# Kernel tuning notes

Measured on AMD Instinct MI355X. Metric: run time of the kernel, lower is better.

## Reference

```python
import jax, jax.numpy as jnp
import numpy as np

B, S, D_MODEL, D_K, D_V = 8, 2048, 1024, 512, 512


def setup_inputs() -> dict:
    key = jax.random.key(0)
    ks = jax.random.split(key, 7)
    sq = jax.random.normal(ks[0], (B, S, D_MODEL), dtype=jnp.float32)
    skv = jax.random.normal(ks[1], (B, S, D_MODEL), dtype=jnp.float32)
    q_pad = jax.random.uniform(ks[2], (B, S)) < 0.1
    kv_pad = jax.random.uniform(ks[3], (B, S)) < 0.1
    Wq = jax.random.normal(ks[4], (D_MODEL, D_K), dtype=jnp.float32) * (D_MODEL ** -0.5)
    Wk = jax.random.normal(ks[5], (D_MODEL, D_K), dtype=jnp.float32) * (D_MODEL ** -0.5)
    Wv = jax.random.normal(ks[6], (D_MODEL, D_V), dtype=jnp.float32) * (D_MODEL ** -0.5)
    return {
        "source_query": sq,
        "source_key_value": skv,
        "source_query_padding_mask": q_pad,
        "source_key_value_padding_mask": kv_pad,
        "Wq": Wq,
        "Wk": Wk,
        "Wv": Wv,
    }


def reference(source_query, source_key_value, source_query_padding_mask,
              source_key_value_padding_mask, Wq, Wk, Wv):
    neg_inf = jnp.float32(-jnp.inf)
    q = source_query @ Wq          # [B,Sq,d_k]
    k = source_key_value @ Wk      # [B,Sk,d_k]
    v = source_key_value @ Wv      # [B,Sk,d_v]
    scale = jnp.float32(D_K) ** -0.5
    scores = jnp.einsum("bqd,bkd->bqk", q, k) * scale  # [B,Sq,Sk]
    # query padding mask broadcast along key dim, kv padding mask along query dim
    pad = source_query_padding_mask[:, :, None] | source_key_value_padding_mask[:, None, :]
    scores = jnp.where(pad, neg_inf, scores)
    # causal mask (masked=True): positions above diagonal blocked
    Sq = scores.shape[1]
    causal = jnp.tril(jnp.ones((Sq, Sq), dtype=bool))
    scores = jnp.where(causal[None, :, :], scores, neg_inf)
    attn = jax.nn.softmax(scores, axis=-1)
    # fully-masked rows produce NaN -> zero (matches torch nan masked_fill)
    attn = jnp.where(jnp.isnan(attn), jnp.float32(0.0), attn)
    # dropout p=0.0 (eval): identity
    out = jnp.einsum("bqk,bkv->bqv", attn, v)  # [B,Sq,d_v]
    return out
```

## Files before the change

kernel.cpp:

```cpp
#include <hip/hip_runtime.h>

typedef unsigned short u16;
typedef unsigned int   u32;
typedef __attribute__((ext_vector_type(4))) float  f32x4;
typedef __attribute__((ext_vector_type(8))) __bf16 bf16x8;

#define BATCH 8
#define SEQ   2048
#define DMODEL 1024
#define DK    512
#define DV    512
#define SCALE 0.044194173824159216f

__device__ __forceinline__ u16 f2bf(float f) {
  u32 u = __float_as_uint(f);
  return (u16)((u + 0x7fffu + ((u >> 16) & 1u)) >> 16);
}

__device__ __forceinline__ bool read_mask(const void* p, int idx, int mode) {
  if (mode == 1) return ((const unsigned char*)p)[idx] != 0;
  if (mode == 2) return ((const float*)p)[idx] != 0.0f;
  return ((const int*)p)[idx] != 0;
}

__device__ __forceinline__ void gl_lds16(const u16* g, u16* l) {
  __builtin_amdgcn_global_load_lds(
      (const __attribute__((address_space(1))) u32*)g,
      (__attribute__((address_space(3))) u32*)l, 16, 0, 0);
}

__global__ void detect_mode(const int* __restrict__ qp, int* __restrict__ flag) {
  __shared__ int f;
  if (threadIdx.x == 0) f = 0;
  __syncthreads();
  int local = 0;
  for (int i = threadIdx.x; i < 4096; i += 256) {
    int v = qp[i];
    if (v == 0x3F800000) local |= 2;
    else if (v != 0 && v != 1 && v != -1) local |= 1;
  }
  if (local) atomicOr(&f, local);
  __syncthreads();
  if (threadIdx.x == 0) {
    int m = 0;
    if (f & 2) m = 2; else if (f & 1) m = 1;
    *flag = m;
  }
}

__global__ __launch_bounds__(256) void wt_transpose(const float* __restrict__ W0,
                                                    const float* __restrict__ W1,
                                                    const float* __restrict__ W2,
                                                    u16* __restrict__ dst) {
  const float* W = (blockIdx.z == 0) ? W0 : (blockIdx.z == 1) ? W1 : W2;
  u16* out = dst + (size_t)blockIdx.z * (DK * DMODEL);
  __shared__ float T[32][33];
  int k0 = blockIdx.x * 32, n0 = blockIdx.y * 32;
  int tx = threadIdx.x, ty = threadIdx.y;
#pragma unroll
  for (int i = 0; i < 4; ++i) {
    int r = ty + i * 8;
    T[r][tx] = W[(size_t)(k0 + r) * DK + n0 + tx];
  }
  __syncthreads();
#pragma unroll
  for (int i = 0; i < 4; ++i) {
    int r = ty + i * 8;
    out[(size_t)(n0 + r) * DMODEL + k0 + tx] = f2bf(T[tx][r]);
  }
}

__global__ __launch_bounds__(256) void convert_bf16(const float* __restrict__ src,
                                                    u16* __restrict__ dst) {
  int i = (blockIdx.x * 256 + threadIdx.x) * 8;
  f32x4 a = *(const f32x4*)(src + i);
  f32x4 b = *(const f32x4*)(src + i + 4);
  uint4 o;
  o.x = (u32)f2bf(a[0]) | ((u32)f2bf(a[1]) << 16);
  o.y = (u32)f2bf(a[2]) | ((u32)f2bf(a[3]) << 16);
  o.z = (u32)f2bf(b[0]) | ((u32)f2bf(b[1]) << 16);
  o.w = (u32)f2bf(b[2]) | ((u32)f2bf(b[3]) << 16);
  *(uint4*)(dst + i) = o;
}

__global__ __launch_bounds__(256, 3) void proj_gemm(const u16* __restrict__ A,
                                                    const u16* __restrict__ Wt_base,
                                                    int z0, u16* __restrict__ dst0,
                                                    u16* __restrict__ dst1) {
  int z = z0 + blockIdx.z;
  const u16* Wt = Wt_base + (size_t)z * (DK * DMODEL);
  u16* dst = (z == 2) ? dst1 : dst0;
  int n0 = blockIdx.x * 128, m0 = blockIdx.y * 128;

  __shared__ __align__(16) u16 As[128 * 64];
  __shared__ __align__(16) u16 Bs[128 * 64];

  int tid = threadIdx.x, lane = tid & 63, w = tid >> 6;
  int wm = w & 1, wn = w >> 1;
  int l15 = lane & 15, lg = lane >> 4;
  int r3 = lane >> 3, c7 = lane & 7;
  int csw = c7 ^ r3;

  f32x4 acc[4][4];
#pragma unroll
  for (int m = 0; m < 4; ++m)
#pragma unroll
    for (int n = 0; n < 4; ++n) acc[m][n] = (f32x4)0.0f;

  for (int k0 = 0; k0 < DMODEL; k0 += 64) {
    __syncthreads();
#pragma unroll
    for (int u = 0; u < 4; ++u) {
      int t = w * 4 + u;
      gl_lds16(A  + (size_t)(m0 + t * 8 + r3) * DMODEL + k0 + csw * 8, &As[t * 512]);
      gl_lds16(Wt + (size_t)(n0 + t * 8 + r3) * DMODEL + k0 + csw * 8, &Bs[t * 512]);
    }
    __syncthreads();
#pragma unroll
    for (int ks = 0; ks < 2; ++ks) {
      bf16x8 af[4], bfv[4];
#pragma unroll
      for (int m = 0; m < 4; ++m) {
        int row = wm * 64 + m * 16 + l15;
        af[m] = *(const bf16x8*)&As[row * 64 + (((ks * 4 + lg) ^ (l15 & 7)) * 8)];
      }
#pragma unroll
      for (int n = 0; n < 4; ++n) {
        int row = wn * 64 + n * 16 + l15;
        bfv[n] = *(const bf16x8*)&Bs[row * 64 + (((ks * 4 + lg) ^ (l15 & 7)) * 8)];
      }
#pragma unroll
      for (int m = 0; m < 4; ++m)
#pragma unroll
        for (int n = 0; n < 4; ++n)
          acc[m][n] = __builtin_amdgcn_mfma_f32_16x16x32_bf16(af[m], bfv[n], acc[m][n], 0, 0, 0);
    }
  }

  if (z != 2) {
#pragma unroll
    for (int m = 0; m < 4; ++m) {
      int rowb = m0 + wm * 64 + m * 16;
#pragma unroll
      for (int n = 0; n < 4; ++n) {
        int col = n0 + wn * 64 + n * 16 + l15;
        size_t base = (size_t)(rowb >> 4) * 8192 + (size_t)(col >> 5) * 512 + (col & 31);
#pragma unroll
        for (int r = 0; r < 4; ++r)
          dst[base + (lg * 4 + r) * 32] = f2bf(acc[m][n][r]);
      }
    }
  } else {
#pragma unroll
    for (int m = 0; m < 4; ++m) {
      int row0 = m0 + wm * 64 + m * 16 + lg * 4;
      int b = row0 >> 11, s0 = row0 & 2047;
#pragma unroll
      for (int n = 0; n < 4; ++n) {
        int dv = n0 + wn * 64 + n * 16 + l15;
        size_t off = (size_t)b * (SEQ * DV) + (size_t)(dv >> 4) * 32768 +
                     (size_t)(s0 >> 5) * 512 + (dv & 15) * 32 + (s0 & 31);
        u16 tmp[4] __attribute__((aligned(8)));
#pragma unroll
        for (int r = 0; r < 4; ++r) tmp[r] = f2bf(acc[m][n][r]);
        *(uint2*)&dst[off] = *(const uint2*)tmp;
      }
    }
  }
}

__global__ __launch_bounds__(512, 4) void attn_kernel(
    const u16* __restrict__ Qf, const u16* __restrict__ Kf,
    const u16* __restrict__ Vf, const void* __restrict__ qpad,
    const void* __restrict__ kvpad, const int* __restrict__ flag,
    float* __restrict__ out) {
  __shared__ __align__(16) u16 Qs[32 * 512];
  __shared__ __align__(16) u16 Pbuf[32 * 72];
  __shared__ float partm[32 * 4];
  __shared__ float partl[32 * 4];

  int tid = threadIdx.x;
  int lane = tid & 63, w = tid >> 6;
  int l15 = lane & 15, lg = lane >> 4;
  int wk = w & 3;
  int m  = w >> 2;
  int bi = blockIdx.x;
  int b = bi & 7, j = bi >> 3;
  int c = j & 31, h = j >> 5;
  int qt = ((c ^ h) & 1) ? (63 - c) : c;
  int q0 = qt * 32;
  int mode = *flag;
  int lanoff = l15 * 32 + lg * 8;

  const u16* Qb = Qf + (size_t)b * (SEQ * DK);
  const u16* Kb = Kf + (size_t)b * (SEQ * DK);
  const u16* Vb = Vf + (size_t)b * (SEQ * DV);

  {
    const u16* qsrc = Qb + (size_t)qt * 16384 + lane * 8;
#pragma unroll
    for (int u = 0; u < 4; ++u) {
      int i = w * 4 + u;
      gl_lds16(qsrc + i * 512, &Qs[i * 512]);
    }
  }

  f32x4 o[2][4];
#pragma unroll
  for (int mf = 0; mf < 2; ++mf)
#pragma unroll
    for (int n = 0; n < 4; ++n) o[mf][n] = (f32x4)0.0f;

  float mo[2][4], lsum[4];
#pragma unroll
  for (int mf = 0; mf < 2; ++mf)
#pragma unroll
    for (int r = 0; r < 4; ++r) mo[mf][r] = -1e38f;
#pragma unroll
  for (int r = 0; r < 4; ++r) lsum[r] = 0.0f;

  int nkt = (q0 + 95) >> 6;
  __syncthreads();

  for (int kt = 0; kt < nkt; ++kt) {
    int k0 = kt * 64;
    int key = k0 + wk * 16 + l15;
    bool kvm = read_mask(kvpad, b * SEQ + key, mode);

    f32x4 sa = (f32x4)0.0f, sb = (f32x4)0.0f;
    {
      const u16* kp = Kb + (size_t)((k0 >> 4) + wk) * 8192 + lanoff;
      const u16* qp = &Qs[m * 8192 + lanoff];
#pragma unroll
      for (int ks = 0; ks < 16; ks += 2) {
        bf16x8 qv0 = *(const bf16x8*)(qp + ks * 512);
        bf16x8 kv0 = *(const bf16x8*)(kp + ks * 512);
        bf16x8 qv1 = *(const bf16x8*)(qp + (ks + 1) * 512);
        bf16x8 kv1 = *(const bf16x8*)(kp + (ks + 1) * 512);
        sa = __builtin_amdgcn_mfma_f32_16x16x32_bf16(qv0, kv0, sa, 0, 0, 0);
        sb = __builtin_amdgcn_mfma_f32_16x16x32_bf16(qv1, kv1, sb, 0, 0, 0);
      }
    }

    float sv[4];
#pragma unroll
    for (int r = 0; r < 4; ++r) {
      int qrow = q0 + m * 16 + lg * 4 + r;
      float x = (sa[r] + sb[r]) * SCALE;
      sv[r] = (kvm || key > qrow) ? -__builtin_inff() : x;
    }

    float wmax[4];
#pragma unroll
    for (int r = 0; r < 4; ++r) wmax[r] = sv[r];
#pragma unroll
    for (int d = 1; d < 16; d <<= 1)
#pragma unroll
      for (int r = 0; r < 4; ++r) wmax[r] = fmaxf(wmax[r], __shfl_xor(wmax[r], d));
    if (l15 == 0) {
#pragma unroll
      for (int r = 0; r < 4; ++r) partm[(m * 16 + lg * 4 + r) * 4 + wk] = wmax[r];
    }
    __syncthreads();

    float al[2][4];
#pragma unroll
    for (int mf = 0; mf < 2; ++mf)
#pragma unroll
      for (int r = 0; r < 4; ++r) {
        int row = mf * 16 + lg * 4 + r;
        float tm = fmaxf(fmaxf(partm[row * 4 + 0], partm[row * 4 + 1]),
                         fmaxf(partm[row * 4 + 2], partm[row * 4 + 3]));
        float mn = fmaxf(mo[mf][r], fmaxf(tm, -1e38f));
        al[mf][r] = __expf(mo[mf][r] - mn);
        mo[mf][r] = mn;
      }
    float ws[4];
#pragma unroll
    for (int r = 0; r < 4; ++r) {
      int row = m * 16 + lg * 4 + r;
      float p = __expf(sv[r] - mo[m][r]);
      Pbuf[row * 72 + wk * 16 + l15] = f2bf(p);
      ws[r] = p;
    }
#pragma unroll
    for (int d = 1; d < 16; d <<= 1)
#pragma unroll
      for (int r = 0; r < 4; ++r) ws[r] += __shfl_xor(ws[r], d);
#pragma unroll
    for (int r = 0; r < 4; ++r) lsum[r] = lsum[r] * al[m][r] + ws[r];
    __syncthreads();

#pragma unroll
    for (int mf = 0; mf < 2; ++mf)
#pragma unroll
      for (int n = 0; n < 4; ++n)
#pragma unroll
        for (int r = 0; r < 4; ++r) o[mf][n][r] *= al[mf][r];

    {
      bf16x8 pa0[2], pa1[2];
#pragma unroll
      for (int ks = 0; ks < 2; ++ks) {
        pa0[ks] = *(const bf16x8*)&Pbuf[l15 * 72 + ks * 32 + lg * 8];
        pa1[ks] = *(const bf16x8*)&Pbuf[(16 + l15) * 72 + ks * 32 + lg * 8];
      }
      const u16* vp = Vb + (size_t)(w * 4) * 32768 + (size_t)(k0 >> 5) * 512 + lanoff;
#pragma unroll
      for (int n = 0; n < 4; ++n) {
#pragma unroll
        for (int ks = 0; ks < 2; ++ks) {
          bf16x8 bv = *(const bf16x8*)(vp + (size_t)n * 32768 + ks * 512);
          o[0][n] = __builtin_amdgcn_mfma_f32_16x16x32_bf16(pa0[ks], bv, o[0][n], 0, 0, 0);
          o[1][n] = __builtin_amdgcn_mfma_f32_16x16x32_bf16(pa1[ks], bv, o[1][n], 0, 0, 0);
        }
      }
    }
  }

  if (l15 == 0) {
#pragma unroll
    for (int r = 0; r < 4; ++r) partl[(m * 16 + lg * 4 + r) * 4 + wk] = lsum[r];
  }
  __syncthreads();
  {
    float f[2][4];
#pragma unroll
    for (int mf = 0; mf < 2; ++mf)
#pragma unroll
      for (int r = 0; r < 4; ++r) {
        int row = mf * 16 + lg * 4 + r;
        float l = partl[row * 4 + 0] + partl[row * 4 + 1] +
                  partl[row * 4 + 2] + partl[row * 4 + 3];
        bool qp = read_mask(qpad, b * SEQ + q0 + row, mode);
        f[mf][r] = (l > 0.0f && !qp) ? 1.0f / l : 0.0f;
      }
#pragma unroll
    for (int mf = 0; mf < 2; ++mf)
#pragma unroll
      for (int n = 0; n < 4; ++n) {
        int dv = w * 64 + n * 16 + l15;
#pragma unroll
        for (int r = 0; r < 4; ++r) {
          int row = mf * 16 + lg * 4 + r;
          out[(size_t)(b * SEQ + q0 + row) * DV + dv] = o[mf][n][r] * f[mf][r];
        }
      }
  }
}

extern "C" void kernel_launch(void* const* d_in, const int* in_sizes, int n_in,
                              void* d_out, int out_size, void* d_ws, size_t ws_size,
                              hipStream_t stream) {
  const float* sq  = (const float*)d_in[0];
  const float* skv = (const float*)d_in[1];
  const void* qp   = d_in[2];
  const void* kvp  = d_in[3];
  const float* Wq  = (const float*)d_in[4];
  const float* Wk  = (const float*)d_in[5];
  const float* Wv  = (const float*)d_in[6];
  char* ws = (char*)d_ws;

  u16* Abf = (u16*)ws;
  u16* Qf  = (u16*)(ws + 33554432);
  u16* Kf  = (u16*)(ws + 50331648);
  u16* Vf  = (u16*)(ws + 67108864);
  u16* Wt  = (u16*)(ws + 83886080);
  int* flag = (int*)(ws + 87031808);

  wt_transpose<<<dim3(32, 16, 3), dim3(32, 8, 1), 0, stream>>>(Wq, Wk, Wv, Wt);
  detect_mode<<<1, 256, 0, stream>>>((const int*)qp, flag);

  convert_bf16<<<8192, 256, 0, stream>>>(sq, Abf);
  proj_gemm<<<dim3(4, 128, 1), dim3(256), 0, stream>>>(Abf, Wt, 0, Qf, Qf);

  convert_bf16<<<8192, 256, 0, stream>>>(skv, Abf);
  proj_gemm<<<dim3(4, 128, 2), dim3(256), 0, stream>>>(Abf, Wt, 1, Kf, Vf);

  attn_kernel<<<dim3(512), dim3(512), 0, stream>>>(Qf, Kf, Vf, qp, kvp, flag,
                                                   (float*)d_out);
}
```

Baseline: 447.6 us.

## Restructure attention into 1024-thread blocks with 128-key tiles and paired query tiles

Block size goes from 512 to 1024 threads, and the grid halves to 256 blocks. Each block now processes two query tiles, (63-c) then c, in two passes to balance causal work. Key tiles grow from 64 to 128 keys, split over 8 waves, and Q fragments are held in registers instead of staged in LDS. The aim is to halve the number of barrier-separated iterations per query tile and drop the Q shared-memory round trip. The cost is much higher register pressure (16 bf16x8 Q fragments per lane), only 256 blocks which may underfill the CUs, and more masked work on the diagonal tile.

```diff
diff --git a/kernel.cpp b/kernel.cpp
--- a/kernel.cpp
+++ b/kernel.cpp
@@ -169,26 +169,24 @@
   }
 }
 
-__global__ __launch_bounds__(512, 4) void attn_kernel(
+__global__ __launch_bounds__(1024) void attn_kernel(
     const u16* __restrict__ Qf, const u16* __restrict__ Kf,
     const u16* __restrict__ Vf, const void* __restrict__ qpad,
     const void* __restrict__ kvpad, const int* __restrict__ flag,
     float* __restrict__ out) {
-  __shared__ __align__(16) u16 Qs[32 * 512];
-  __shared__ __align__(16) u16 Pbuf[32 * 72];
-  __shared__ float partm[32 * 4];
-  __shared__ float partl[32 * 4];
+  __shared__ __align__(16) u16 Pbuf[32 * 136];
+  __shared__ __align__(16) float partm[32 * 8];
+  __shared__ __align__(16) float partl[32 * 8];
 
   int tid = threadIdx.x;
   int lane = tid & 63, w = tid >> 6;
   int l15 = lane & 15, lg = lane >> 4;
-  int wk = w & 3;
-  int m  = w >> 2;
+  int wk = w & 7;
+  int mS = w >> 3;
+  int mf = w & 1;
+  int dq = w >> 1;
   int bi = blockIdx.x;
-  int b = bi & 7, j = bi >> 3;
-  int c = j & 31, h = j >> 5;
-  int qt = ((c ^ h) & 1) ? (63 - c) : c;
-  int q0 = qt * 32;
+  int b = bi & 7, c = bi >> 3;
   int mode = *flag;
   int lanoff = l15 * 32 + lg * 8;
 
@@ -196,156 +194,156 @@
   const u16* Kb = Kf + (size_t)b * (SEQ * DK);
   const u16* Vb = Vf + (size_t)b * (SEQ * DV);
 
-  {
-    const u16* qsrc = Qb + (size_t)qt * 16384 + lane * 8;
-#pragma unroll
-    for (int u = 0; u < 4; ++u) {
-      int i = w * 4 + u;
-      gl_lds16(qsrc + i * 512, &Qs[i * 512]);
-    }
-  }
-
-  f32x4 o[2][4];
-#pragma unroll
-  for (int mf = 0; mf < 2; ++mf)
-#pragma unroll
-    for (int n = 0; n < 4; ++n) o[mf][n] = (f32x4)0.0f;
-
-  float mo[2][4], lsum[4];
-#pragma unroll
-  for (int mf = 0; mf < 2; ++mf)
-#pragma unroll
-    for (int r = 0; r < 4; ++r) mo[mf][r] = -1e38f;
-#pragma unroll
-  for (int r = 0; r < 4; ++r) lsum[r] = 0.0f;
-
-  int nkt = (q0 + 95) >> 6;
-  __syncthreads();
-
-  for (int kt = 0; kt < nkt; ++kt) {
-    int k0 = kt * 64;
-    int key = k0 + wk * 16 + l15;
-    bool kvm = read_mask(kvpad, b * SEQ + key, mode);
-
-    f32x4 sa = (f32x4)0.0f, sb = (f32x4)0.0f;
+#pragma unroll 1
+  for (int pass = 0; pass < 2; ++pass) {
+    int qt = pass ? c : (63 - c);
+    int q0 = qt * 32;
+
+    bf16x8 qf[16];
     {
-      const u16* kp = Kb + (size_t)((k0 >> 4) + wk) * 8192 + lanoff;
-      const u16* qp = &Qs[m * 8192 + lanoff];
-#pragma unroll
-      for (int ks = 0; ks < 16; ks += 2) {
-        bf16x8 qv0 = *(const bf16x8*)(qp + ks * 512);
-        bf16x8 kv0 = *(const bf16x8*)(kp + ks * 512);
-        bf16x8 qv1 = *(const bf16x8*)(qp + (ks + 1) * 512);
-        bf16x8 kv1 = *(const bf16x8*)(kp + (ks + 1) * 512);
-        sa = __builtin_amdgcn_mfma_f32_16x16x32_bf16(qv0, kv0, sa, 0, 0, 0);
-        sb = __builtin_amdgcn_mfma_f32_16x16x32_bf16(qv1, kv1, sb, 0, 0, 0);
-      }
-    }
-
-    float sv[4];
-#pragma unroll
-    for (int r = 0; r < 4; ++r) {
-      int qrow = q0 + m * 16 + lg * 4 + r;
-      float x = (sa[r] + sb[r]) * SCALE;
-      sv[r] = (kvm || key > qrow) ? -__builtin_inff() : x;
-    }
-
-    float wmax[4];
-#pragma unroll
-    for (int r = 0; r < 4; ++r) wmax[r] = sv[r];
-#pragma unroll
-    for (int d = 1; d < 16; d <<= 1)
-#pragma unroll
-      for (int r = 0; r < 4; ++r) wmax[r] = fmaxf(wmax[r], __shfl_xor(wmax[r], d));
+      const u16* qp = Qb + (size_t)(qt * 2 + mS) * 8192 + lanoff;
+#pragma unroll
+      for (int ks = 0; ks < 16; ++ks) qf[ks] = *(const bf16x8*)(qp + ks * 512);
+    }
+
+    f32x4 o[4];
+#pragma unroll
+    for (int n = 0; n < 4; ++n) o[n] = (f32x4)0.0f;
+
+    float mo[2][4], lsum[4];
+#pragma unroll
+    for (int mfi = 0; mfi < 2; ++mfi)
+#pragma unroll
+      for (int r = 0; r < 4; ++r) mo[mfi][r] = -1e38f;
+#pragma unroll
+    for (int r = 0; r < 4; ++r) lsum[r] = 0.0f;
+
+    int nkt = (q0 + 159) >> 7;
+
+    for (int kt = 0; kt < nkt; ++kt) {
+      int k0 = kt << 7;
+      int key = k0 + wk * 16 + l15;
+      bool kvm = read_mask(kvpad, b * SEQ + key, mode);
+
+      f32x4 sa = (f32x4)0.0f, sb = (f32x4)0.0f;
+      {
+        const u16* kp = Kb + (size_t)(kt * 8 + wk) * 8192 + lanoff;
+#pragma unroll
+        for (int ks = 0; ks < 16; ks += 2) {
+          bf16x8 kv0 = *(const bf16x8*)(kp + ks * 512);
+          bf16x8 kv1 = *(const bf16x8*)(kp + (ks + 1) * 512);
+          sa = __builtin_amdgcn_mfma_f32_16x16x32_bf16(qf[ks], kv0, sa, 0, 0, 0);
+          sb = __builtin_amdgcn_mfma_f32_16x16x32_bf16(qf[ks + 1], kv1, sb, 0, 0, 0);
+        }
+      }
+
+      float sv[4];
+#pragma unroll
+      for (int r = 0; r < 4; ++r) {
+        int qrow = q0 + mS * 16 + lg * 4 + r;
+        float x = (sa[r] + sb[r]) * SCALE;
+        sv[r] = (kvm || key > qrow) ? -__builtin_inff() : x;
+      }
+
+      float wmax[4];
+#pragma unroll
+      for (int r = 0; r < 4; ++r) wmax[r] = sv[r];
+#pragma unroll
+      for (int d = 1; d < 16; d <<= 1)
+#pragma unroll
+        for (int r = 0; r < 4; ++r) wmax[r] = fmaxf(wmax[r], __shfl_xor(wmax[r], d));
+      if (l15 == 0) {
+#pragma unroll
+        for (int r = 0; r < 4; ++r) partm[(mS * 16 + lg * 4 + r) * 8 + wk] = wmax[r];
+      }
+      __syncthreads();
+
+      float al[2][4];
+#pragma unroll
+      for (int mfi = 0; mfi < 2; ++mfi)
+#pragma unroll
+        for (int r = 0; r < 4; ++r) {
+          int row = mfi * 16 + lg * 4 + r;
+          f32x4 p0 = *(const f32x4*)&partm[row * 8];
+          f32x4 p1 = *(const f32x4*)&partm[row * 8 + 4];
+          float tm = fmaxf(fmaxf(fmaxf(p0[0], p0[1]), fmaxf(p0[2], p0[3])),
+                           fmaxf(fmaxf(p1[0], p1[1]), fmaxf(p1[2], p1[3])));
+          float mn = fmaxf(mo[mfi][r], fmaxf(tm, -1e38f));
+          al[mfi][r] = __expf(mo[mfi][r] - mn);
+          mo[mfi][r] = mn;
+        }
+      float ws[4];
+#pragma unroll
+      for (int r = 0; r < 4; ++r) {
+        int row = mS * 16 + lg * 4 + r;
+        float mS_m = mS ? mo[1][r] : mo[0][r];
+        float p = __expf(sv[r] - mS_m);
+        Pbuf[row * 136 + wk * 16 + l15] = f2bf(p);
+        ws[r] = p;
+      }
+#pragma unroll
+      for (int d = 1; d < 16; d <<= 1)
+#pragma unroll
+        for (int r = 0; r < 4; ++r) ws[r] += __shfl_xor(ws[r], d);
+#pragma unroll
+      for (int r = 0; r < 4; ++r) {
+        float alS = mS ? al[1][r] : al[0][r];
+        lsum[r] = lsum[r] * alS + ws[r];
+      }
+      __syncthreads();
+
+#pragma unroll
+      for (int n = 0; n < 4; ++n)
+#pragma unroll
+        for (int r = 0; r < 4; ++r) {
+          float alF = mf ? al[1][r] : al[0][r];
+          o[n][r] *= alF;
+        }
+
+      {
+        bf16x8 pa[4];
+#pragma unroll
+        for (int ks = 0; ks < 4; ++ks)
+          pa[ks] = *(const bf16x8*)&Pbuf[(mf * 16 + l15) * 136 + ks * 32 + lg * 8];
+        const u16* vp = Vb + (size_t)(dq * 4) * 32768 + (size_t)(kt * 4) * 512 + lanoff;
+#pragma unroll
+        for (int n = 0; n < 4; ++n) {
+#pragma unroll
+          for (int ks = 0; ks < 4; ++ks) {
+            bf16x8 bv = *(const bf16x8*)(vp + (size_t)n * 32768 + ks * 512);
+            o[n] = __builtin_amdgcn_mfma_f32_16x16x32_bf16(pa[ks], bv, o[n], 0, 0, 0);
+          }
+        }
+      }
+    }
+
     if (l15 == 0) {
 #pragma unroll
-      for (int r = 0; r < 4; ++r) partm[(m * 16 + lg * 4 + r) * 4 + wk] = wmax[r];
+      for (int r = 0; r < 4; ++r) partl[(mS * 16 + lg * 4 + r) * 8 + wk] = lsum[r];
     }
     __syncthreads();
-
-    float al[2][4];
-#pragma unroll
-    for (int mf = 0; mf < 2; ++mf)
+    {
+      float f[4];
 #pragma unroll
       for (int r = 0; r < 4; ++r) {
         int row = mf * 16 + lg * 4 + r;
-        float tm = fmaxf(fmaxf(partm[row * 4 + 0], partm[row * 4 + 1]),
-                         fmaxf(partm[row * 4 + 2], partm[row * 4 + 3]));
-        float mn = fmaxf(mo[mf][r], fmaxf(tm, -1e38f));
-        al[mf][r] = __expf(mo[mf][r] - mn);
-        mo[mf][r] = mn;
-      }
-    float ws[4];
-#pragma unroll
-    for (int r = 0; r < 4; ++r) {
-      int row = m * 16 + lg * 4 + r;
-      float p = __expf(sv[r] - mo[m][r]);
-      Pbuf[row * 72 + wk * 16 + l15] = f2bf(p);
-      ws[r] = p;
-    }
-#pragma unroll
-    for (int d = 1; d < 16; d <<= 1)
-#pragma unroll
-      for (int r = 0; r < 4; ++r) ws[r] += __shfl_xor(ws[r], d);
-#pragma unroll
-    for (int r = 0; r < 4; ++r) lsum[r] = lsum[r] * al[m][r] + ws[r];
-    __syncthreads();
-
-#pragma unroll
-    for (int mf = 0; mf < 2; ++mf)
-#pragma unroll
-      for (int n = 0; n < 4; ++n)
-#pragma unroll
-        for (int r = 0; r < 4; ++r) o[mf][n][r] *= al[mf][r];
-
-    {
-      bf16x8 pa0[2], pa1[2];
-#pragma unroll
-      for (int ks = 0; ks < 2; ++ks) {
-        pa0[ks] = *(const bf16x8*)&Pbuf[l15 * 72 + ks * 32 + lg * 8];
-        pa1[ks] = *(const bf16x8*)&Pbuf[(16 + l15) * 72 + ks * 32 + lg * 8];
-      }
-      const u16* vp = Vb + (size_t)(w * 4) * 32768 + (size_t)(k0 >> 5) * 512 + lanoff;
+        f32x4 a = *(const f32x4*)&partl[row * 8];
+        f32x4 b2 = *(const f32x4*)&partl[row * 8 + 4];
+        float l = (a[0] + a[1] + a[2] + a[3]) + (b2[0] + b2[1] + b2[2] + b2[3]);
+        bool qp = read_mask(qpad, b * SEQ + q0 + row, mode);
+        f[r] = (l > 0.0f && !qp) ? 1.0f / l : 0.0f;
+      }
 #pragma unroll
       for (int n = 0; n < 4; ++n) {
-#pragma unroll
-        for (int ks = 0; ks < 2; ++ks) {
-          bf16x8 bv = *(const bf16x8*)(vp + (size_t)n * 32768 + ks * 512);
-          o[0][n] = __builtin_amdgcn_mfma_f32_16x16x32_bf16(pa0[ks], bv, o[0][n], 0, 0, 0);
-          o[1][n] = __builtin_amdgcn_mfma_f32_16x16x32_bf16(pa1[ks], bv, o[1][n], 0, 0, 0);
-        }
-      }
-    }
-  }
-
-  if (l15 == 0) {
-#pragma unroll
-    for (int r = 0; r < 4; ++r) partl[(m * 16 + lg * 4 + r) * 4 + wk] = lsum[r];
-  }
-  __syncthreads();
-  {
-    float f[2][4];
-#pragma unroll
-    for (int mf = 0; mf < 2; ++mf)
-#pragma unroll
-      for (int r = 0; r < 4; ++r) {
-        int row = mf * 16 + lg * 4 + r;
-        float l = partl[row * 4 + 0] + partl[row * 4 + 1] +
-                  partl[row * 4 + 2] + partl[row * 4 + 3];
-        bool qp = read_mask(qpad, b * SEQ + q0 + row, mode);
-        f[mf][r] = (l > 0.0f && !qp) ? 1.0f / l : 0.0f;
-      }
-#pragma unroll
-    for (int mf = 0; mf < 2; ++mf)
-#pragma unroll
-      for (int n = 0; n < 4; ++n) {
-        int dv = w * 64 + n * 16 + l15;
+        int dv = dq * 64 + n * 16 + l15;
 #pragma unroll
         for (int r = 0; r < 4; ++r) {
           int row = mf * 16 + lg * 4 + r;
-          out[(size_t)(b * SEQ + q0 + row) * DV + dv] = o[mf][n][r] * f[mf][r];
-        }
-      }
+          out[(size_t)(b * SEQ + q0 + row) * DV + dv] = o[n][r] * f[r];
+        }
+      }
+    }
+    __syncthreads();
   }
 }
 
@@ -377,6 +375,6 @@
   convert_bf16<<<8192, 256, 0, stream>>>(skv, Abf);
   proj_gemm<<<dim3(4, 128, 2), dim3(256), 0, stream>>>(Abf, Wt, 1, Kf, Vf);
 
-  attn_kernel<<<dim3(512), dim3(512), 0, stream>>>(Qf, Kf, Vf, qp, kvp, flag,
-                                                   (float*)d_out);
-}
+  attn_kernel<<<dim3(256), dim3(1024), 0, stream>>>(Qf, Kf, Vf, qp, kvp, flag,
+                                                    (float*)d_out);
+}
```

Measured after the change: 538.5 us. 1.2x slower.

## Pair causal query tiles per block and swizzle Q in LDS, prefetch V

Applied to the files above, without the earlier changes.

The attention kernel now launches 256 blocks, and each block processes two query tiles in sequence, a long one (63-c) and then a short one (c), so every block does an equal amount of causal work. Q is loaded into LDS with an XOR swizzle to reduce bank conflicts, and V fragments are loaded into registers right after the QK MFMAs so their latency overlaps the softmax. The rescale factor is computed once per row and shared through LDS instead of being computed redundantly, and the partial max/sum reads use vector LDS loads. With half the blocks on a 256-CU part, occupancy and latency hiding may drop.

```diff
diff --git a/kernel.cpp b/kernel.cpp
--- a/kernel.cpp
+++ b/kernel.cpp
@@ -176,176 +176,187 @@
     float* __restrict__ out) {
   __shared__ __align__(16) u16 Qs[32 * 512];
   __shared__ __align__(16) u16 Pbuf[32 * 72];
-  __shared__ float partm[32 * 4];
-  __shared__ float partl[32 * 4];
+  __shared__ __align__(16) float partm[32 * 4];
+  __shared__ __align__(16) float partl[32 * 4];
+  __shared__ __align__(16) float ald[32];
 
   int tid = threadIdx.x;
   int lane = tid & 63, w = tid >> 6;
   int l15 = lane & 15, lg = lane >> 4;
   int wk = w & 3;
-  int m  = w >> 2;
+  int mS = w >> 2;
   int bi = blockIdx.x;
-  int b = bi & 7, j = bi >> 3;
-  int c = j & 31, h = j >> 5;
-  int qt = ((c ^ h) & 1) ? (63 - c) : c;
-  int q0 = qt * 32;
+  int b = bi & 7, c = bi >> 3;
   int mode = *flag;
   int lanoff = l15 * 32 + lg * 8;
+  int qswz = (((l15 * 4 + lg) ^ (l15 >> 1)) * 8);
+  int sswz = ((lane ^ ((lane >> 3) & 7)) * 8);
 
   const u16* Qb = Qf + (size_t)b * (SEQ * DK);
   const u16* Kb = Kf + (size_t)b * (SEQ * DK);
   const u16* Vb = Vf + (size_t)b * (SEQ * DV);
 
-  {
-    const u16* qsrc = Qb + (size_t)qt * 16384 + lane * 8;
-#pragma unroll
-    for (int u = 0; u < 4; ++u) {
-      int i = w * 4 + u;
-      gl_lds16(qsrc + i * 512, &Qs[i * 512]);
-    }
-  }
-
-  f32x4 o[2][4];
-#pragma unroll
-  for (int mf = 0; mf < 2; ++mf)
-#pragma unroll
-    for (int n = 0; n < 4; ++n) o[mf][n] = (f32x4)0.0f;
-
-  float mo[2][4], lsum[4];
-#pragma unroll
-  for (int mf = 0; mf < 2; ++mf)
-#pragma unroll
-    for (int r = 0; r < 4; ++r) mo[mf][r] = -1e38f;
-#pragma unroll
-  for (int r = 0; r < 4; ++r) lsum[r] = 0.0f;
-
-  int nkt = (q0 + 95) >> 6;
-  __syncthreads();
-
-  for (int kt = 0; kt < nkt; ++kt) {
-    int k0 = kt * 64;
-    int key = k0 + wk * 16 + l15;
-    bool kvm = read_mask(kvpad, b * SEQ + key, mode);
-
-    f32x4 sa = (f32x4)0.0f, sb = (f32x4)0.0f;
+#pragma unroll 1
+  for (int pass = 0; pass < 2; ++pass) {
+    int qt = pass ? c : (63 - c);
+    int q0 = qt * 32;
+
     {
-      const u16* kp = Kb + (size_t)((k0 >> 4) + wk) * 8192 + lanoff;
-      const u16* qp = &Qs[m * 8192 + lanoff];
-#pragma unroll
-      for (int ks = 0; ks < 16; ks += 2) {
-        bf16x8 qv0 = *(const bf16x8*)(qp + ks * 512);
-        bf16x8 kv0 = *(const bf16x8*)(kp + ks * 512);
-        bf16x8 qv1 = *(const bf16x8*)(qp + (ks + 1) * 512);
-        bf16x8 kv1 = *(const bf16x8*)(kp + (ks + 1) * 512);
-        sa = __builtin_amdgcn_mfma_f32_16x16x32_bf16(qv0, kv0, sa, 0, 0, 0);
-        sb = __builtin_amdgcn_mfma_f32_16x16x32_bf16(qv1, kv1, sb, 0, 0, 0);
-      }
-    }
-
-    float sv[4];
-#pragma unroll
-    for (int r = 0; r < 4; ++r) {
-      int qrow = q0 + m * 16 + lg * 4 + r;
-      float x = (sa[r] + sb[r]) * SCALE;
-      sv[r] = (kvm || key > qrow) ? -__builtin_inff() : x;
-    }
-
-    float wmax[4];
-#pragma unroll
-    for (int r = 0; r < 4; ++r) wmax[r] = sv[r];
-#pragma unroll
-    for (int d = 1; d < 16; d <<= 1)
-#pragma unroll
-      for (int r = 0; r < 4; ++r) wmax[r] = fmaxf(wmax[r], __shfl_xor(wmax[r], d));
+      const u16* qsrc = Qb + (size_t)qt * 16384 + sswz;
+#pragma unroll
+      for (int u = 0; u < 8; ++u) {
+        int i = w * 8 + u;
+        gl_lds16(qsrc + i * 512, &Qs[i * 512]);
+      }
+    }
+
+    f32x4 o[2][4];
+#pragma unroll
+    for (int mf = 0; mf < 2; ++mf)
+#pragma unroll
+      for (int n = 0; n < 4; ++n) o[mf][n] = (f32x4)0.0f;
+
+    float mo[4], lsum[4];
+#pragma unroll
+    for (int r = 0; r < 4; ++r) { mo[r] = -1e38f; lsum[r] = 0.0f; }
+
+    int nkt = (q0 + 95) >> 6;
+    __syncthreads();
+
+    for (int kt = 0; kt < nkt; ++kt) {
+      int key = (kt << 6) + wk * 16 + l15;
+      bool kvm = read_mask(kvpad, b * SEQ + key, mode);
+
+      f32x4 sa = (f32x4)0.0f, sb = (f32x4)0.0f;
+      {
+        const u16* kp = Kb + (size_t)(kt * 4 + wk) * 8192 + lanoff;
+        const u16* qp = &Qs[mS * 8192 + qswz];
+#pragma unroll
+        for (int ks = 0; ks < 16; ks += 2) {
+          bf16x8 qv0 = *(const bf16x8*)(qp + ks * 512);
+          bf16x8 kv0 = *(const bf16x8*)(kp + ks * 512);
+          bf16x8 qv1 = *(const bf16x8*)(qp + (ks + 1) * 512);
+          bf16x8 kv1 = *(const bf16x8*)(kp + (ks + 1) * 512);
+          sa = __builtin_amdgcn_mfma_f32_16x16x32_bf16(qv0, kv0, sa, 0, 0, 0);
+          sb = __builtin_amdgcn_mfma_f32_16x16x32_bf16(qv1, kv1, sb, 0, 0, 0);
+        }
+      }
+
+      bf16x8 vpre[8];
+      {
+        const u16* vp = Vb + (size_t)(w * 4) * 32768 + (size_t)(kt * 2) * 512 + lanoff;
+#pragma unroll
+        for (int n = 0; n < 4; ++n)
+#pragma unroll
+          for (int ks2 = 0; ks2 < 2; ++ks2)
+            vpre[n * 2 + ks2] = *(const bf16x8*)(vp + (size_t)n * 32768 + ks2 * 512);
+      }
+
+      float sv[4];
+#pragma unroll
+      for (int r = 0; r < 4; ++r) {
+        int qrow = q0 + mS * 16 + lg * 4 + r;
+        float x = (sa[r] + sb[r]) * SCALE;
+        sv[r] = (kvm || key > qrow) ? -__builtin_inff() : x;
+      }
+
+      float wmax[4];
+#pragma unroll
+      for (int r = 0; r < 4; ++r) wmax[r] = sv[r];
+#pragma unroll
+      for (int d = 1; d < 16; d <<= 1)
+#pragma unroll
+        for (int r = 0; r < 4; ++r) wmax[r] = fmaxf(wmax[r], __shfl_xor(wmax[r], d));
+      if (l15 == 0) {
+#pragma unroll
+        for (int r = 0; r < 4; ++r) partm[(mS * 16 + lg * 4 + r) * 4 + wk] = wmax[r];
+      }
+      __syncthreads();
+
+      float al[4], ws[4];
+#pragma unroll
+      for (int r = 0; r < 4; ++r) {
+        int row = mS * 16 + lg * 4 + r;
+        f32x4 pm = *(const f32x4*)&partm[row * 4];
+        float tm = fmaxf(fmaxf(pm[0], pm[1]), fmaxf(pm[2], pm[3]));
+        float mn = fmaxf(mo[r], fmaxf(tm, -1e38f));
+        al[r] = __expf(mo[r] - mn);
+        mo[r] = mn;
+        float p = __expf(sv[r] - mn);
+        Pbuf[row * 72 + wk * 16 + l15] = f2bf(p);
+        ws[r] = p;
+      }
+#pragma unroll
+      for (int d = 1; d < 16; d <<= 1)
+#pragma unroll
+        for (int r = 0; r < 4; ++r) ws[r] += __shfl_xor(ws[r], d);
+#pragma unroll
+      for (int r = 0; r < 4; ++r) lsum[r] = lsum[r] * al[r] + ws[r];
+      if (wk == 0 && l15 == 0) {
+#pragma unroll
+        for (int r = 0; r < 4; ++r) ald[mS * 16 + lg * 4 + r] = al[r];
+      }
+      __syncthreads();
+
+      float ar[2][4];
+#pragma unroll
+      for (int mf = 0; mf < 2; ++mf)
+#pragma unroll
+        for (int r = 0; r < 4; ++r) ar[mf][r] = ald[mf * 16 + lg * 4 + r];
+#pragma unroll
+      for (int mf = 0; mf < 2; ++mf)
+#pragma unroll
+        for (int n = 0; n < 4; ++n)
+#pragma unroll
+          for (int r = 0; r < 4; ++r) o[mf][n][r] *= ar[mf][r];
+
+      {
+        bf16x8 pa0[2], pa1[2];
+#pragma unroll
+        for (int ks2 = 0; ks2 < 2; ++ks2) {
+          pa0[ks2] = *(const bf16x8*)&Pbuf[l15 * 72 + ks2 * 32 + lg * 8];
+          pa1[ks2] = *(const bf16x8*)&Pbuf[(16 + l15) * 72 + ks2 * 32 + lg * 8];
+        }
+#pragma unroll
+        for (int n = 0; n < 4; ++n)
+#pragma unroll
+          for (int ks2 = 0; ks2 < 2; ++ks2) {
+            o[0][n] = __builtin_amdgcn_mfma_f32_16x16x32_bf16(pa0[ks2], vpre[n * 2 + ks2], o[0][n], 0, 0, 0);
+            o[1][n] = __builtin_amdgcn_mfma_f32_16x16x32_bf16(pa1[ks2], vpre[n * 2 + ks2], o[1][n], 0, 0, 0);
+          }
+      }
+    }
+
     if (l15 == 0) {
 #pragma unroll
-      for (int r = 0; r < 4; ++r) partm[(m * 16 + lg * 4 + r) * 4 + wk] = wmax[r];
-    }
-    __syncthreads();
-
-    float al[2][4];
-#pragma unroll
-    for (int mf = 0; mf < 2; ++mf)
-#pragma unroll
-      for (int r = 0; r < 4; ++r) {
-        int row = mf * 16 + lg * 4 + r;
-        float tm = fmaxf(fmaxf(partm[row * 4 + 0], partm[row * 4 + 1]),
-                         fmaxf(partm[row * 4 + 2], partm[row * 4 + 3]));
-        float mn = fmaxf(mo[mf][r], fmaxf(tm, -1e38f));
-        al[mf][r] = __expf(mo[mf][r] - mn);
-        mo[mf][r] = mn;
-      }
-    float ws[4];
-#pragma unroll
-    for (int r = 0; r < 4; ++r) {
-      int row = m * 16 + lg * 4 + r;
-      float p = __expf(sv[r] - mo[m][r]);
-      Pbuf[row * 72 + wk * 16 + l15] = f2bf(p);
-      ws[r] = p;
-    }
-#pragma unroll
-    for (int d = 1; d < 16; d <<= 1)
-#pragma unroll
-      for (int r = 0; r < 4; ++r) ws[r] += __shfl_xor(ws[r], d);
-#pragma unroll
-    for (int r = 0; r < 4; ++r) lsum[r] = lsum[r] * al[m][r] + ws[r];
-    __syncthreads();
-
-#pragma unroll
-    for (int mf = 0; mf < 2; ++mf)
-#pragma unroll
-      for (int n = 0; n < 4; ++n)
-#pragma unroll
-        for (int r = 0; r < 4; ++r) o[mf][n][r] *= al[mf][r];
-
+      for (int r = 0; r < 4; ++r) partl[(mS * 16 + lg * 4 + r) * 4 + wk] = lsum[r];
+    }
+    __syncthreads();
     {
-      bf16x8 pa0[2], pa1[2];
-#pragma unroll
-      for (int ks = 0; ks < 2; ++ks) {
-        pa0[ks] = *(const bf16x8*)&Pbuf[l15 * 72 + ks * 32 + lg * 8];
-        pa1[ks] = *(const bf16x8*)&Pbuf[(16 + l15) * 72 + ks * 32 + lg * 8];
-      }
-      const u16* vp = Vb + (size_t)(w * 4) * 32768 + (size_t)(k0 >> 5) * 512 + lanoff;
-#pragma unroll
-      for (int n = 0; n < 4; ++n) {
-#pragma unroll
-        for (int ks = 0; ks < 2; ++ks) {
-          bf16x8 bv = *(const bf16x8*)(vp + (size_t)n * 32768 + ks * 512);
-          o[0][n] = __builtin_amdgcn_mfma_f32_16x16x32_bf16(pa0[ks], bv, o[0][n], 0, 0, 0);
-          o[1][n] = __builtin_amdgcn_mfma_f32_16x16x32_bf16(pa1[ks], bv, o[1][n], 0, 0, 0);
-        }
-      }
-    }
-  }
-
-  if (l15 == 0) {
-#pragma unroll
-    for (int r = 0; r < 4; ++r) partl[(m * 16 + lg * 4 + r) * 4 + wk] = lsum[r];
-  }
-  __syncthreads();
-  {
-    float f[2][4];
-#pragma unroll
-    for (int mf = 0; mf < 2; ++mf)
-#pragma unroll
-      for (int r = 0; r < 4; ++r) {
-        int row = mf * 16 + lg * 4 + r;
-        float l = partl[row * 4 + 0] + partl[row * 4 + 1] +
-                  partl[row * 4 + 2] + partl[row * 4 + 3];
-        bool qp = read_mask(qpad, b * SEQ + q0 + row, mode);
-        f[mf][r] = (l > 0.0f && !qp) ? 1.0f / l : 0.0f;
-      }
-#pragma unroll
-    for (int mf = 0; mf < 2; ++mf)
-#pragma unroll
-      for (int n = 0; n < 4; ++n) {
-        int dv = w * 64 + n * 16 + l15;
+      float f[2][4];
+#pragma unroll
+      for (int mf = 0; mf < 2; ++mf)
 #pragma unroll
         for (int r = 0; r < 4; ++r) {
           int row = mf * 16 + lg * 4 + r;
-          out[(size_t)(b * SEQ + q0 + row) * DV + dv] = o[mf][n][r] * f[mf][r];
+          f32x4 a = *(const f32x4*)&partl[row * 4];
+          float l = (a[0] + a[1]) + (a[2] + a[3]);
+          bool qp = read_mask(qpad, b * SEQ + q0 + row, mode);
+          f[mf][r] = (l > 0.0f && !qp) ? 1.0f / l : 0.0f;
         }
-      }
+#pragma unroll
+      for (int mf = 0; mf < 2; ++mf)
+#pragma unroll
+        for (int n = 0; n < 4; ++n) {
+          int dv = w * 64 + n * 16 + l15;
+#pragma unroll
+          for (int r = 0; r < 4; ++r) {
+            int row = mf * 16 + lg * 4 + r;
+            out[(size_t)(b * SEQ + q0 + row) * DV + dv] = o[mf][n][r] * f[mf][r];
+          }
+        }
+    }
+    __syncthreads();
   }
 }
 
@@ -377,6 +388,6 @@
   convert_bf16<<<8192, 256, 0, stream>>>(skv, Abf);
   proj_gemm<<<dim3(4, 128, 2), dim3(256), 0, stream>>>(Abf, Wt, 1, Kf, Vf);
 
-  attn_kernel<<<dim3(512), dim3(512), 0, stream>>>(Qf, Kf, Vf, qp, kvp, flag,
+  attn_kernel<<<dim3(256), dim3(512), 0, stream>>>(Qf, Kf, Vf, qp, kvp, flag,
                                                    (float*)d_out);
 }
```

After: 477.4 us. +6.7%, slower.
